# Performance work log

Hardware: AMD Instinct MI355X
Metric: run time of the kernel (lower is better)

## Reference

```python
import jax, jax.numpy as jnp
import numpy as np

C = 256  # num_channels
N = 524288  # number of 2D query points


def _linear_params(key, fan_in, fan_out):
    # torch nn.Linear default init: U(-1/sqrt(fan_in), 1/sqrt(fan_in))
    kw, kb = jax.random.split(key)
    bound = 1.0 / np.sqrt(fan_in)
    W = jax.random.uniform(kw, (fan_in, fan_out), jnp.float32, -bound, bound)
    b = jax.random.uniform(kb, (fan_out,), jnp.float32, -bound, bound)
    return W, b


def setup_inputs() -> dict:
    key = jax.random.key(0)
    k_uv, k0, k1, k2, k3 = jax.random.split(key, 5)
    uv = jax.random.uniform(k_uv, (N, 2), jnp.float32)
    W_in, b_in = _linear_params(k0, 4, C)
    W_h0, b_h0 = _linear_params(k1, C, C)
    W_h1, b_h1 = _linear_params(k2, C, C)
    W_out, b_out = _linear_params(k3, C, 3)
    return {
        "uv": uv,
        "W_in": W_in, "b_in": b_in,
        "W_h0": W_h0, "b_h0": b_h0,
        "W_h1": W_h1, "b_h1": b_h1,
        "W_out": W_out, "b_out": b_out,
    }


def reference(uv, W_in, b_in, W_h0, b_h0, W_h1, b_h1, W_out, b_out):
    # NOTE: in the original, `encoded = 2*pi*uv` is overwritten, so the
    # effective encoding is simply [cos(uv), sin(uv)] -> last dim 4.
    encoded = jnp.concatenate([jnp.cos(uv), jnp.sin(uv)], axis=-1)  # [N, 4]
    h = jax.nn.relu(encoded @ W_in + b_in)   # [N, C]
    h = jax.nn.relu(h @ W_h0 + b_h0)          # [N, C]
    h = jax.nn.relu(h @ W_h1 + b_h1)          # [N, C]
    out = jax.nn.sigmoid(h @ W_out + b_out)   # [N, 3]
    return out
```

## Files before the change

### kernel.cpp

```cpp
#include <hip/hip_runtime.h>
#include <hip/hip_bf16.h>
#include <math.h>

#define CCH 256
#define MT  64
#define ROWE 264
#define TPB 512

typedef __attribute__((ext_vector_type(8))) short short8;
typedef __attribute__((ext_vector_type(4))) short short4v;
typedef __attribute__((ext_vector_type(4))) float f32x4;

__device__ unsigned short g_T0[CCH * CCH];
__device__ unsigned short g_T1[CCH * CCH];
__device__ unsigned short g_Wo[16 * CCH];

__device__ __forceinline__ unsigned short f2bf(float f) {
  unsigned u = __float_as_uint(f);
  u += 0x7fffu + ((u >> 16) & 1u);
  return (unsigned short)(u >> 16);
}

__global__ void transpose_w(const float* __restrict__ W0,
                            const float* __restrict__ W1) {
  __shared__ float tile[32][33];
  const float* src = blockIdx.z ? W1 : W0;
  unsigned short* dst = blockIdx.z ? g_T1 : g_T0;
  const int tx = threadIdx.x, ty = threadIdx.y;
  const int k0 = blockIdx.y * 32, n0 = blockIdx.x * 32;
#pragma unroll
  for (int r = 0; r < 4; ++r)
    tile[ty + r * 8][tx] = src[(k0 + ty + r * 8) * CCH + n0 + tx];
  __syncthreads();
#pragma unroll
  for (int r = 0; r < 4; ++r) {
    const int n = n0 + ty + r * 8;
    dst[n * CCH + k0 + tx] = f2bf(tile[tx][ty + r * 8]);
  }
}

__global__ void prep_wo(const float* __restrict__ W_out) {
  const int k = threadIdx.x;
#pragma unroll
  for (int j = 0; j < 16; ++j)
    g_Wo[j * CCH + k] = (j < 3) ? f2bf(W_out[k * 3 + j]) : (unsigned short)0;
}

__device__ __forceinline__ void load_w(short8 w[2][8],
                                       const unsigned short* __restrict__ Wt,
                                       int wv, int l16, int lk8) {
#pragma unroll
  for (int kk = 0; kk < 8; ++kk) {
    const int k = kk * 32 + lk8 * 8;
    w[0][kk] = *(const short8*)&Wt[(wv * 32 + l16) * CCH + k];
    w[1][kk] = *(const short8*)&Wt[(wv * 32 + 16 + l16) * CCH + k];
  }
}

__device__ __forceinline__ void layer_mfma(
    const unsigned short (*__restrict__ src)[ROWE],
    unsigned short (*__restrict__ dst)[ROWE],
    const short8 w[2][8],
    const float* __restrict__ bias,
    int wv, int l16, int lk8) {
  f32x4 acc[4][2];
#pragma unroll
  for (int mt = 0; mt < 4; ++mt)
#pragma unroll
    for (int nt = 0; nt < 2; ++nt)
      acc[mt][nt] = (f32x4){0.f, 0.f, 0.f, 0.f};

#pragma unroll
  for (int kk = 0; kk < 8; ++kk) {
    const int k = kk * 32 + lk8 * 8;
#pragma unroll
    for (int mt = 0; mt < 4; ++mt) {
      const short8 a = *(const short8*)&src[mt * 16 + l16][k];
      acc[mt][0] = __builtin_amdgcn_mfma_f32_16x16x32_bf16(w[0][kk], a, acc[mt][0], 0, 0, 0);
      acc[mt][1] = __builtin_amdgcn_mfma_f32_16x16x32_bf16(w[1][kk], a, acc[mt][1], 0, 0, 0);
    }
  }

#pragma unroll
  for (int nt = 0; nt < 2; ++nt) {
    const int ch0 = wv * 32 + nt * 16 + lk8 * 4;
    const f32x4 bv = *(const f32x4*)&bias[ch0];
#pragma unroll
    for (int mt = 0; mt < 4; ++mt) {
      const int pt = mt * 16 + l16;
      short4v pk;
#pragma unroll
      for (int i = 0; i < 4; ++i)
        pk[i] = (short)f2bf(fmaxf(acc[mt][nt][i] + bv[i], 0.0f));
      *(short4v*)&dst[pt][ch0] = pk;
    }
  }
}

__global__ __launch_bounds__(TPB, 4) void nerf_fused(
    const float* __restrict__ uv,
    const float* __restrict__ W_in, const float* __restrict__ b_in,
    const float* __restrict__ b_h0, const float* __restrict__ b_h1,
    const float* __restrict__ b_out,
    float* __restrict__ out) {
  __shared__ unsigned short hA[MT][ROWE];
  __shared__ unsigned short hB[MT][ROWE];

  const int tid = threadIdx.x;
  const long n0 = (long)blockIdx.x * MT;
  const int wv = tid >> 6, ln = tid & 63;
  const int l16 = ln & 15, lk8 = ln >> 4;

  short8 w[2][8];
  load_w(w, g_T0, wv, l16, lk8);
  asm volatile("" ::: "memory");

  {
    const int p = tid >> 3;
    const int t7 = tid & 7;
    const float u = uv[(n0 + p) * 2 + 0];
    const float v = uv[(n0 + p) * 2 + 1];
    const float e0 = __cosf(u), e1 = __cosf(v), e2 = __sinf(u), e3 = __sinf(v);
#pragma unroll
    for (int j = 0; j < 8; ++j) {
      const int c = t7 * 4 + j * 32;
      const f32x4 w0 = *(const f32x4*)&W_in[0 * CCH + c];
      const f32x4 w1 = *(const f32x4*)&W_in[1 * CCH + c];
      const f32x4 w2 = *(const f32x4*)&W_in[2 * CCH + c];
      const f32x4 w3 = *(const f32x4*)&W_in[3 * CCH + c];
      const f32x4 bb = *(const f32x4*)&b_in[c];
      short4v pk;
#pragma unroll
      for (int i = 0; i < 4; ++i) {
        const float x = bb[i] + e0 * w0[i] + e1 * w1[i] + e2 * w2[i] + e3 * w3[i];
        pk[i] = (short)f2bf(fmaxf(x, 0.0f));
      }
      *(short4v*)&hA[p][c] = pk;
    }
  }
  __syncthreads();

  layer_mfma(hA, hB, w, b_h0, wv, l16, lk8);
  load_w(w, g_T1, wv, l16, lk8);
  asm volatile("" ::: "memory");
  __syncthreads();
  layer_mfma(hB, hA, w, b_h1, wv, l16, lk8);
  __syncthreads();

  if (wv < 4) {
    f32x4 oacc = (f32x4){0.f, 0.f, 0.f, 0.f};
#pragma unroll
    for (int kk = 0; kk < 8; ++kk) {
      const int k = kk * 32 + lk8 * 8;
      const short8 wo = *(const short8*)&g_Wo[l16 * CCH + k];
      const short8 hb = *(const short8*)&hA[wv * 16 + l16][k];
      oacc = __builtin_amdgcn_mfma_f32_16x16x32_bf16(wo, hb, oacc, 0, 0, 0);
    }
    if (lk8 == 0) {
      const long pt = n0 + wv * 16 + l16;
#pragma unroll
      for (int i = 0; i < 3; ++i)
        out[pt * 3 + i] = 1.f / (1.f + __expf(-(oacc[i] + b_out[i])));
    }
  }
}

extern "C" void kernel_launch(void* const* d_in, const int* in_sizes, int n_in,
                              void* d_out, int out_size, void* d_ws, size_t ws_size,
                              hipStream_t stream) {
  const float* uv    = (const float*)d_in[0];
  const float* W_in  = (const float*)d_in[1];
  const float* b_in  = (const float*)d_in[2];
  const float* W_h0  = (const float*)d_in[3];
  const float* b_h0  = (const float*)d_in[4];
  const float* W_h1  = (const float*)d_in[5];
  const float* b_h1  = (const float*)d_in[6];
  const float* W_out = (const float*)d_in[7];
  const float* b_out = (const float*)d_in[8];

  const int N = in_sizes[0] / 2;

  transpose_w<<<dim3(8, 8, 2), dim3(32, 8), 0, stream>>>(W_h0, W_h1);
  prep_wo<<<1, CCH, 0, stream>>>(W_out);
  nerf_fused<<<dim3(N / MT), dim3(TPB), 0, stream>>>(
      uv, W_in, b_in, b_h0, b_h1, b_out, (float*)d_out);
}
```

Before: 418.7 us.

## Halve point tile, stream weights from global, raise occupancy with packed bf16 cvt

Shrinks the per-block tile from 64 to 32 points and stops keeping each wave's weight slice in registers. Weights are now read from global/L2 inside the k-loop, which frees VGPRs and lets launch bounds request 8 blocks per CU instead of 4. It also swaps the manual float-to-bf16 rounding for the hardware v_cvt_pk_bf16_f32 instruction. The trade-off is that each block now fetches the full weight matrices again, which doubles weight traffic per point and adds load latency inside the MFMA loop.

New measurement: 640.4 us. +53.0%, slower.

```diff
diff --git a/kernel.cpp b/kernel.cpp
--- a/kernel.cpp
+++ b/kernel.cpp
@@ -3,13 +3,13 @@
 #include <math.h>
 
 #define CCH 256
-#define MT  64
+#define MT  32
 #define ROWE 264
 #define TPB 512
 
 typedef __attribute__((ext_vector_type(8))) short short8;
-typedef __attribute__((ext_vector_type(4))) short short4v;
 typedef __attribute__((ext_vector_type(4))) float f32x4;
+typedef __attribute__((ext_vector_type(2))) unsigned int uint2v;
 
 __device__ unsigned short g_T0[CCH * CCH];
 __device__ unsigned short g_T1[CCH * CCH];
@@ -19,6 +19,12 @@
   unsigned u = __float_as_uint(f);
   u += 0x7fffu + ((u >> 16) & 1u);
   return (unsigned short)(u >> 16);
+}
+
+__device__ __forceinline__ unsigned cvtpk(float lo, float hi) {
+  unsigned r;
+  asm("v_cvt_pk_bf16_f32 %0, %1, %2" : "=v"(r) : "v"(lo), "v"(hi));
+  return r;
 }
 
 __global__ void transpose_w(const float* __restrict__ W0,
@@ -46,39 +52,34 @@
     g_Wo[j * CCH + k] = (j < 3) ? f2bf(W_out[k * 3 + j]) : (unsigned short)0;
 }
 
-__device__ __forceinline__ void load_w(short8 w[2][8],
-                                       const unsigned short* __restrict__ Wt,
-                                       int wv, int l16, int lk8) {
-#pragma unroll
-  for (int kk = 0; kk < 8; ++kk) {
-    const int k = kk * 32 + lk8 * 8;
-    w[0][kk] = *(const short8*)&Wt[(wv * 32 + l16) * CCH + k];
-    w[1][kk] = *(const short8*)&Wt[(wv * 32 + 16 + l16) * CCH + k];
-  }
-}
-
 __device__ __forceinline__ void layer_mfma(
     const unsigned short (*__restrict__ src)[ROWE],
     unsigned short (*__restrict__ dst)[ROWE],
-    const short8 w[2][8],
+    const unsigned short* __restrict__ Wt,
     const float* __restrict__ bias,
     int wv, int l16, int lk8) {
-  f32x4 acc[4][2];
+  f32x4 acc[2][2];
 #pragma unroll
-  for (int mt = 0; mt < 4; ++mt)
+  for (int mt = 0; mt < 2; ++mt)
 #pragma unroll
     for (int nt = 0; nt < 2; ++nt)
       acc[mt][nt] = (f32x4){0.f, 0.f, 0.f, 0.f};
 
+  const unsigned short* w0p = &Wt[(wv * 32 + l16) * CCH + lk8 * 8];
+  const unsigned short* w1p = w0p + 16 * CCH;
+  const unsigned short* a0p = &src[l16][lk8 * 8];
+
 #pragma unroll
   for (int kk = 0; kk < 8; ++kk) {
-    const int k = kk * 32 + lk8 * 8;
-#pragma unroll
-    for (int mt = 0; mt < 4; ++mt) {
-      const short8 a = *(const short8*)&src[mt * 16 + l16][k];
-      acc[mt][0] = __builtin_amdgcn_mfma_f32_16x16x32_bf16(w[0][kk], a, acc[mt][0], 0, 0, 0);
-      acc[mt][1] = __builtin_amdgcn_mfma_f32_16x16x32_bf16(w[1][kk], a, acc[mt][1], 0, 0, 0);
-    }
+    const int k = kk * 32;
+    const short8 w0 = *(const short8*)&w0p[k];
+    const short8 w1 = *(const short8*)&w1p[k];
+    const short8 a0 = *(const short8*)&a0p[k];
+    const short8 a1 = *(const short8*)&a0p[16 * ROWE + k];
+    acc[0][0] = __builtin_amdgcn_mfma_f32_16x16x32_bf16(w0, a0, acc[0][0], 0, 0, 0);
+    acc[0][1] = __builtin_amdgcn_mfma_f32_16x16x32_bf16(w1, a0, acc[0][1], 0, 0, 0);
+    acc[1][0] = __builtin_amdgcn_mfma_f32_16x16x32_bf16(w0, a1, acc[1][0], 0, 0, 0);
+    acc[1][1] = __builtin_amdgcn_mfma_f32_16x16x32_bf16(w1, a1, acc[1][1], 0, 0, 0);
   }
 
 #pragma unroll
@@ -86,18 +87,19 @@
     const int ch0 = wv * 32 + nt * 16 + lk8 * 4;
     const f32x4 bv = *(const f32x4*)&bias[ch0];
 #pragma unroll
-    for (int mt = 0; mt < 4; ++mt) {
+    for (int mt = 0; mt < 2; ++mt) {
       const int pt = mt * 16 + l16;
-      short4v pk;
-#pragma unroll
-      for (int i = 0; i < 4; ++i)
-        pk[i] = (short)f2bf(fmaxf(acc[mt][nt][i] + bv[i], 0.0f));
-      *(short4v*)&dst[pt][ch0] = pk;
+      uint2v pk;
+      pk[0] = cvtpk(fmaxf(acc[mt][nt][0] + bv[0], 0.f),
+                    fmaxf(acc[mt][nt][1] + bv[1], 0.f));
+      pk[1] = cvtpk(fmaxf(acc[mt][nt][2] + bv[2], 0.f),
+                    fmaxf(acc[mt][nt][3] + bv[3], 0.f));
+      *(uint2v*)&dst[pt][ch0] = pk;
     }
   }
 }
 
-__global__ __launch_bounds__(TPB, 4) void nerf_fused(
+__global__ __launch_bounds__(TPB, 8) void nerf_fused(
     const float* __restrict__ uv,
     const float* __restrict__ W_in, const float* __restrict__ b_in,
     const float* __restrict__ b_h0, const float* __restrict__ b_h1,
@@ -111,43 +113,38 @@
   const int wv = tid >> 6, ln = tid & 63;
   const int l16 = ln & 15, lk8 = ln >> 4;
 
-  short8 w[2][8];
-  load_w(w, g_T0, wv, l16, lk8);
-  asm volatile("" ::: "memory");
-
   {
-    const int p = tid >> 3;
-    const int t7 = tid & 7;
+    const int p = tid >> 4;
+    const int t15 = tid & 15;
     const float u = uv[(n0 + p) * 2 + 0];
     const float v = uv[(n0 + p) * 2 + 1];
     const float e0 = __cosf(u), e1 = __cosf(v), e2 = __sinf(u), e3 = __sinf(v);
 #pragma unroll
-    for (int j = 0; j < 8; ++j) {
-      const int c = t7 * 4 + j * 32;
+    for (int j = 0; j < 4; ++j) {
+      const int c = t15 * 4 + j * 64;
       const f32x4 w0 = *(const f32x4*)&W_in[0 * CCH + c];
       const f32x4 w1 = *(const f32x4*)&W_in[1 * CCH + c];
       const f32x4 w2 = *(const f32x4*)&W_in[2 * CCH + c];
       const f32x4 w3 = *(const f32x4*)&W_in[3 * CCH + c];
       const f32x4 bb = *(const f32x4*)&b_in[c];
-      short4v pk;
+      float x[4];
 #pragma unroll
-      for (int i = 0; i < 4; ++i) {
-        const float x = bb[i] + e0 * w0[i] + e1 * w1[i] + e2 * w2[i] + e3 * w3[i];
-        pk[i] = (short)f2bf(fmaxf(x, 0.0f));
-      }
-      *(short4v*)&hA[p][c] = pk;
+      for (int i = 0; i < 4; ++i)
+        x[i] = fmaxf(bb[i] + e0 * w0[i] + e1 * w1[i] + e2 * w2[i] + e3 * w3[i], 0.f);
+      uint2v pk;
+      pk[0] = cvtpk(x[0], x[1]);
+      pk[1] = cvtpk(x[2], x[3]);
+      *(uint2v*)&hA[p][c] = pk;
     }
   }
   __syncthreads();
 
-  layer_mfma(hA, hB, w, b_h0, wv, l16, lk8);
-  load_w(w, g_T1, wv, l16, lk8);
-  asm volatile("" ::: "memory");
+  layer_mfma(hA, hB, g_T0, b_h0, wv, l16, lk8);
   __syncthreads();
-  layer_mfma(hB, hA, w, b_h1, wv, l16, lk8);
+  layer_mfma(hB, hA, g_T1, b_h1, wv, l16, lk8);
   __syncthreads();
 
-  if (wv < 4) {
+  if (wv < 2) {
     f32x4 oacc = (f32x4){0.f, 0.f, 0.f, 0.f};
 #pragma unroll
     for (int kk = 0; kk < 8; ++kk) {
```
